# Kernel tuning notes

Measured on AMD Instinct MI355X. Metric: run time of the kernel, lower is better.

The kernel has to match this reference:

```python
import jax, jax.numpy as jnp
import numpy as np

TEMPERATURE = 0.1


def setup_inputs() -> dict:
    key = jax.random.key(0)
    k1, k2 = jax.random.split(key)
    B, D = 4096, 128
    z_i = jax.random.normal(k1, (B, D), dtype=jnp.float32)
    z_j = jax.random.normal(k2, (B, D), dtype=jnp.float32)
    return {"z_i": z_i, "z_j": z_j}


def reference(z_i, z_j):
    B = z_i.shape[0]
    n = 2 * B
    z = jnp.concatenate([z_i, z_j], axis=0)            # [2B, D]
    sim = jnp.matmul(z, z.T) / TEMPERATURE             # [2B, 2B]
    # positives: diag(sim, +B) and diag(sim, -B)
    pos = jnp.concatenate([jnp.diagonal(sim, B), jnp.diagonal(sim, -B)])[:, None]  # [2B, 1]
    # negatives: sim with diagonal removed, row-wise -> [2B, 2B-1]
    # strided trick equivalent to sim[~eye].reshape(n, n-1)
    neg = sim.ravel()[:-1].reshape(n - 1, n + 1)[:, 1:].reshape(n, n - 1)
    logits = jnp.concatenate([pos, neg], axis=1)       # [2B, 2B]
    # cross-entropy with labels all zero (positive in column 0)
    loss = jnp.mean(jax.nn.logsumexp(logits, axis=1) - logits[:, 0])
    return loss
```

## Files before the change

kernel.cpp:

```cpp
#include <hip/hip_runtime.h>
#include <hip/hip_bf16.h>
#include <stdint.h>

#define N_TOT  8192
#define BHALF  4096
#define DDIM   128
#define NSPLIT 16

typedef short bf16x8 __attribute__((ext_vector_type(8)));
typedef float f32x4  __attribute__((ext_vector_type(4)));

__device__ __forceinline__ float ex2(float x) { return __builtin_amdgcn_exp2f(x); }

#define SCALE_C 3.798282440185f

__device__ __forceinline__ ushort2 cvt2(float a, float b) {
    __hip_bfloat162 h = __float22bfloat162_rn(make_float2(a, b));
    return *reinterpret_cast<ushort2*>(&h);
}

__device__ __forceinline__ bf16x8 cvt8(float4 lo, float4 hi) {
    union { bf16x8 v; ushort2 u[4]; } r;
    r.u[0] = cvt2(lo.x * SCALE_C, lo.y * SCALE_C);
    r.u[1] = cvt2(lo.z * SCALE_C, lo.w * SCALE_C);
    r.u[2] = cvt2(hi.x * SCALE_C, hi.y * SCALE_C);
    r.u[3] = cvt2(hi.z * SCALE_C, hi.w * SCALE_C);
    return r.v;
}

struct StageRegs { float4 v[4]; };

__device__ __forceinline__ StageRegs stage_load(const float* __restrict__ zi,
                                                const float* __restrict__ zj,
                                                int colBase, int ch, int tid) {
    StageRegs s;
    #pragma unroll
    for (int it = 0; it < 2; ++it) {
        int idx  = it * 512 + tid;
        int col  = idx >> 4, g = idx & 15;
        int gcol = colBase + ch * 64 + col;
        const float* cp = (gcol < BHALF) ? zi + gcol * DDIM
                                         : zj + (gcol - BHALF) * DDIM;
        s.v[it * 2]     = *reinterpret_cast<const float4*>(cp + g * 8);
        s.v[it * 2 + 1] = *reinterpret_cast<const float4*>(cp + g * 8 + 4);
    }
    return s;
}

__device__ __forceinline__ void stage_write(const StageRegs& s, int tid,
                                            unsigned short* buf) {
    #pragma unroll
    for (int it = 0; it < 2; ++it) {
        int idx  = it * 512 + tid;
        int col  = idx >> 4, g = idx & 15;
        int slot = g ^ (col & 7);
        *reinterpret_cast<bf16x8*>(&buf[col * 128 + slot * 8]) =
            cvt8(s.v[it * 2], s.v[it * 2 + 1]);
    }
}

__launch_bounds__(512, 4)
__global__ void k_main(const float* __restrict__ zi, const float* __restrict__ zj,
                       float* __restrict__ pm, float* __restrict__ pl,
                       float* __restrict__ out) {
    if (blockIdx.x == 0 && threadIdx.x == 0) out[0] = 0.f;
    __shared__ unsigned short lds[2][64 * 128];
    const int tid = threadIdx.x;
    const int w = tid >> 6, lane = tid & 63;
    const int q = lane >> 4, ln = lane & 15;
    const int rb = blockIdx.x >> 4, cs = blockIdx.x & 15;
    const int rowBase = rb * 256 + w * 32;
    const int colBase = cs * 512;

    bf16x8 afr[2][4];
    #pragma unroll
    for (int s = 0; s < 2; ++s) {
        int row = rowBase + s * 16 + ln;
        const float* rp = (row < BHALF) ? zi + row * DDIM
                                        : zj + (row - BHALF) * DDIM;
        #pragma unroll
        for (int kc = 0; kc < 4; ++kc) {
            float4 lo = *reinterpret_cast<const float4*>(rp + kc * 32 + q * 8);
            float4 hi = *reinterpret_cast<const float4*>(rp + kc * 32 + q * 8 + 4);
            afr[s][kc] = cvt8(lo, hi);
        }
    }

    float m[2][4], l[2][4];
    #pragma unroll
    for (int s = 0; s < 2; ++s)
        #pragma unroll
        for (int r = 0; r < 4; ++r) { m[s][r] = -1e38f; l[s][r] = 0.f; }

    StageRegs sr = stage_load(zi, zj, colBase, 0, tid);
    stage_write(sr, tid, lds[0]);
    __syncthreads();

    for (int ch = 0; ch < 8; ++ch) {
        const unsigned short* buf = lds[ch & 1];
        if (ch < 7) sr = stage_load(zi, zj, colBase, ch + 1, tid);

        #pragma unroll
        for (int ct2 = 0; ct2 < 2; ++ct2) {
            f32x4 acc[2][2];
            #pragma unroll
            for (int s = 0; s < 2; ++s)
                #pragma unroll
                for (int u = 0; u < 2; ++u) acc[s][u] = (f32x4){0.f, 0.f, 0.f, 0.f};

            #pragma unroll
            for (int u = 0; u < 2; ++u) {
                int ct = ct2 * 2 + u;
                bf16x8 bfr[4];
                #pragma unroll
                for (int kc = 0; kc < 4; ++kc) {
                    int slot = (q + 4 * kc) ^ (ln & 7);
                    bfr[kc] = *reinterpret_cast<const bf16x8*>(
                        &buf[(ct * 16 + ln) * 128 + slot * 8]);
                }
                #pragma unroll
                for (int s = 0; s < 2; ++s)
                    #pragma unroll
                    for (int kc = 0; kc < 4; ++kc)
                        acc[s][u] = __builtin_amdgcn_mfma_f32_16x16x32_bf16(
                            afr[s][kc], bfr[kc], acc[s][u], 0, 0, 0);
            }

            const int c0 = colBase + ch * 64 + ct2 * 32;
            #pragma unroll
            for (int s = 0; s < 2; ++s) {
                const int rt = rowBase + s * 16;
                if (c0 == rt) {
                    #pragma unroll
                    for (int r = 0; r < 4; ++r)
                        if (ln == q * 4 + r) acc[s][0][r] = -__builtin_inff();
                } else if (c0 + 16 == rt) {
                    #pragma unroll
                    for (int r = 0; r < 4; ++r)
                        if (ln == q * 4 + r) acc[s][1][r] = -__builtin_inff();
                }
                #pragma unroll
                for (int r = 0; r < 4; ++r) {
                    float t0 = acc[s][0][r], t1 = acc[s][1][r];
                    float mo = m[s][r];
                    float mn = fmaxf(fmaxf(t0, t1), mo);
                    float sc = ex2(mo - mn);
                    float pv = ex2(t0 - mn) + ex2(t1 - mn);
                    l[s][r] = fmaf(l[s][r], sc, pv);
                    m[s][r] = mn;
                }
            }
        }

        if (ch < 7) stage_write(sr, tid, lds[(ch + 1) & 1]);
        __syncthreads();
    }

    #pragma unroll
    for (int s = 0; s < 2; ++s) {
        #pragma unroll
        for (int r = 0; r < 4; ++r) {
            float mm = m[s][r], ll = l[s][r];
            #pragma unroll
            for (int msk = 1; msk < 16; msk <<= 1) {
                float om = __shfl_xor(mm, msk, 64);
                float ol = __shfl_xor(ll, msk, 64);
                float mn = fmaxf(mm, om);
                ll = ll * ex2(mm - mn) + ol * ex2(om - mn);
                mm = mn;
            }
            if (ln == 0) {
                int row = rowBase + s * 16 + q * 4 + r;
                pm[cs * N_TOT + row] = mm;
                pl[cs * N_TOT + row] = ll;
            }
        }
    }
}

__global__ void k_finish(const float* __restrict__ zi, const float* __restrict__ zj,
                         const float* __restrict__ pm, const float* __restrict__ pl,
                         float* __restrict__ out) {
    int row = blockIdx.x * 256 + threadIdx.x;
    int pr  = row & (BHALF - 1);
    const float4* a = reinterpret_cast<const float4*>(zi + pr * DDIM);
    const float4* b = reinterpret_cast<const float4*>(zj + pr * DDIM);
    float acc = 0.f;
    #pragma unroll
    for (int k = 0; k < 32; ++k) {
        float4 x = a[k], y = b[k];
        acc += x.x * y.x + x.y * y.y + x.z * y.z + x.w * y.w;
    }
    float p  = 10.f * acc;
    float tp = p * 1.4426950408889634f;
    float mm[NSPLIT];
    float M = tp;
    #pragma unroll
    for (int j = 0; j < NSPLIT; ++j) {
        mm[j] = pm[j * N_TOT + row];
        M = fmaxf(M, mm[j]);
    }
    float S = ex2(tp - M);
    #pragma unroll
    for (int j = 0; j < NSPLIT; ++j)
        S += pl[j * N_TOT + row] * ex2(mm[j] - M);
    float lse = (M + __log2f(S)) * 0.6931471805599453f;
    float li  = lse - p;
    #pragma unroll
    for (int msk = 32; msk; msk >>= 1) li += __shfl_xor(li, msk, 64);
    __shared__ float red[4];
    if ((threadIdx.x & 63) == 0) red[threadIdx.x >> 6] = li;
    __syncthreads();
    if (threadIdx.x == 0)
        atomicAdd(out, (red[0] + red[1] + red[2] + red[3]) * (1.f / 8192.f));
}

extern "C" void kernel_launch(void* const* d_in, const int* in_sizes, int n_in,
                              void* d_out, int out_size, void* d_ws, size_t ws_size,
                              hipStream_t stream) {
    const float* zi = (const float*)d_in[0];
    const float* zj = (const float*)d_in[1];
    float* out = (float*)d_out;
    char* ws = (char*)d_ws;

    float* pm = (float*)ws;
    float* pl = pm + NSPLIT * N_TOT;

    hipLaunchKernelGGL(k_main,   dim3(512), dim3(512), 0, stream, zi, zj, pm, pl, out);
    hipLaunchKernelGGL(k_finish, dim3(32),  dim3(256), 0, stream, zi, zj, pm, pl, out);
}
```

Measured before the change: 99.93 us.

## Split columns into 32 chunks and capture positive logits from the main GEMM

Doubles the column split so the main kernel launches 1024 blocks, each covering 256 columns. It raises the launch-bounds occupancy hint to 8 blocks per multiprocessor. Positive-pair logits are now taken from the bf16 MFMA tile when a tile crosses the partner diagonal and written to a buffer, so the finish kernel no longer recomputes the fp32 dot products. The cost is a larger partial-max/sum workspace, a more costly merge over 32 partials, and positives now at bf16 rather than fp32 precision.

```diff
diff --git a/kernel.cpp b/kernel.cpp
--- a/kernel.cpp
+++ b/kernel.cpp
@@ -5,7 +5,7 @@
 #define N_TOT  8192
 #define BHALF  4096
 #define DDIM   128
-#define NSPLIT 16
+#define NSPLIT 32
 
 typedef short bf16x8 __attribute__((ext_vector_type(8)));
 typedef float f32x4  __attribute__((ext_vector_type(4)));
@@ -59,18 +59,18 @@
     }
 }
 
-__launch_bounds__(512, 4)
+__launch_bounds__(512, 8)
 __global__ void k_main(const float* __restrict__ zi, const float* __restrict__ zj,
                        float* __restrict__ pm, float* __restrict__ pl,
-                       float* __restrict__ out) {
+                       float* __restrict__ posb, float* __restrict__ out) {
     if (blockIdx.x == 0 && threadIdx.x == 0) out[0] = 0.f;
     __shared__ unsigned short lds[2][64 * 128];
     const int tid = threadIdx.x;
     const int w = tid >> 6, lane = tid & 63;
     const int q = lane >> 4, ln = lane & 15;
-    const int rb = blockIdx.x >> 4, cs = blockIdx.x & 15;
+    const int rb = blockIdx.x >> 5, cs = blockIdx.x & 31;
     const int rowBase = rb * 256 + w * 32;
-    const int colBase = cs * 512;
+    const int colBase = cs * 256;
 
     bf16x8 afr[2][4];
     #pragma unroll
@@ -96,9 +96,9 @@
     stage_write(sr, tid, lds[0]);
     __syncthreads();
 
-    for (int ch = 0; ch < 8; ++ch) {
+    for (int ch = 0; ch < 4; ++ch) {
         const unsigned short* buf = lds[ch & 1];
-        if (ch < 7) sr = stage_load(zi, zj, colBase, ch + 1, tid);
+        if (ch < 3) sr = stage_load(zi, zj, colBase, ch + 1, tid);
 
         #pragma unroll
         for (int ct2 = 0; ct2 < 2; ++ct2) {
@@ -138,6 +138,16 @@
                     #pragma unroll
                     for (int r = 0; r < 4; ++r)
                         if (ln == q * 4 + r) acc[s][1][r] = -__builtin_inff();
+                }
+                const int prt = rt ^ 4096;
+                if (c0 == prt) {
+                    #pragma unroll
+                    for (int r = 0; r < 4; ++r)
+                        if (ln == q * 4 + r) posb[rt + q * 4 + r] = acc[s][0][r];
+                } else if (c0 + 16 == prt) {
+                    #pragma unroll
+                    for (int r = 0; r < 4; ++r)
+                        if (ln == q * 4 + r) posb[rt + q * 4 + r] = acc[s][1][r];
                 }
                 #pragma unroll
                 for (int r = 0; r < 4; ++r) {
@@ -152,7 +162,7 @@
             }
         }
 
-        if (ch < 7) stage_write(sr, tid, lds[(ch + 1) & 1]);
+        if (ch < 3) stage_write(sr, tid, lds[(ch + 1) & 1]);
         __syncthreads();
     }
 
@@ -178,21 +188,10 @@
     }
 }
 
-__global__ void k_finish(const float* __restrict__ zi, const float* __restrict__ zj,
-                         const float* __restrict__ pm, const float* __restrict__ pl,
-                         float* __restrict__ out) {
-    int row = blockIdx.x * 256 + threadIdx.x;
-    int pr  = row & (BHALF - 1);
-    const float4* a = reinterpret_cast<const float4*>(zi + pr * DDIM);
-    const float4* b = reinterpret_cast<const float4*>(zj + pr * DDIM);
-    float acc = 0.f;
-    #pragma unroll
-    for (int k = 0; k < 32; ++k) {
-        float4 x = a[k], y = b[k];
-        acc += x.x * y.x + x.y * y.y + x.z * y.z + x.w * y.w;
-    }
-    float p  = 10.f * acc;
-    float tp = p * 1.4426950408889634f;
+__global__ void k_finish(const float* __restrict__ pm, const float* __restrict__ pl,
+                         const float* __restrict__ posb, float* __restrict__ out) {
+    int row = blockIdx.x * 128 + threadIdx.x;
+    float tp = posb[row];
     float mm[NSPLIT];
     float M = tp;
     #pragma unroll
@@ -204,15 +203,14 @@
     #pragma unroll
     for (int j = 0; j < NSPLIT; ++j)
         S += pl[j * N_TOT + row] * ex2(mm[j] - M);
-    float lse = (M + __log2f(S)) * 0.6931471805599453f;
-    float li  = lse - p;
+    float li = 0.6931471805599453f * (M + __log2f(S) - tp);
     #pragma unroll
     for (int msk = 32; msk; msk >>= 1) li += __shfl_xor(li, msk, 64);
-    __shared__ float red[4];
+    __shared__ float red[2];
     if ((threadIdx.x & 63) == 0) red[threadIdx.x >> 6] = li;
     __syncthreads();
     if (threadIdx.x == 0)
-        atomicAdd(out, (red[0] + red[1] + red[2] + red[3]) * (1.f / 8192.f));
+        atomicAdd(out, (red[0] + red[1]) * (1.f / 8192.f));
 }
 
 extern "C" void kernel_launch(void* const* d_in, const int* in_sizes, int n_in,
@@ -223,9 +221,10 @@
     float* out = (float*)d_out;
     char* ws = (char*)d_ws;
 
-    float* pm = (float*)ws;
-    float* pl = pm + NSPLIT * N_TOT;
-
-    hipLaunchKernelGGL(k_main,   dim3(512), dim3(512), 0, stream, zi, zj, pm, pl, out);
-    hipLaunchKernelGGL(k_finish, dim3(32),  dim3(256), 0, stream, zi, zj, pm, pl, out);
-}
+    float* pm   = (float*)ws;
+    float* pl   = pm + NSPLIT * N_TOT;
+    float* posb = pl + NSPLIT * N_TOT;
+
+    hipLaunchKernelGGL(k_main,   dim3(1024), dim3(512), 0, stream, zi, zj, pm, pl, posb, out);
+    hipLaunchKernelGGL(k_finish, dim3(64),   dim3(128), 0, stream, pm, pl, posb, out);
+}
```

Result: slower. 295.2 us (+195.4%).
